# Optimization experiments

Hardware: AMD Instinct MI355X
Metric: run time of the kernel (lower is better)

Reference implementation:

```python
import jax, jax.numpy as jnp
import numpy as np

B, S, E, H = 4, 2048, 1024, 16
D = E // H  # head_dim = 64


def setup_inputs() -> dict:
    key0 = jax.random.key(0)
    ks = jax.random.split(key0, 11)
    sc = 1.0 / np.sqrt(E)
    return {
        "query": jax.random.normal(ks[0], (B, S, E), jnp.float32),
        "key": jax.random.normal(ks[1], (B, S, E), jnp.float32),
        "value": jax.random.normal(ks[2], (B, S, E), jnp.float32),
        "Wq": jax.random.normal(ks[3], (E, E), jnp.float32) * sc,
        "bq": jax.random.normal(ks[4], (E,), jnp.float32) * sc,
        "Wk": jax.random.normal(ks[5], (E, E), jnp.float32) * sc,
        "bk": jax.random.normal(ks[6], (E,), jnp.float32) * sc,
        "Wv": jax.random.normal(ks[7], (E, E), jnp.float32) * sc,
        "bv": jax.random.normal(ks[8], (E,), jnp.float32) * sc,
        "Wo": jax.random.normal(ks[9], (E, E), jnp.float32) * sc,
        "bo": jax.random.normal(ks[10], (E,), jnp.float32) * sc,
    }


def reference(query, key, value, Wq, bq, Wk, bk, Wv, bv, Wo, bo):
    b, s, e = query.shape
    q = query @ Wq + bq
    k = key @ Wk + bk
    v = value @ Wv + bv
    # [b, s, E] -> [b, H, s, D]
    qh = q.reshape(b, s, H, D).transpose(0, 2, 1, 3)
    kh = k.reshape(b, s, H, D).transpose(0, 2, 1, 3)
    vh = v.reshape(b, s, H, D).transpose(0, 2, 1, 3)
    energy = jnp.einsum('nhql,nhkl->nhqk', qh, kh)  # [b, H, s, s]
    scale = jnp.asarray(1.0 / np.sqrt(D), energy.dtype)
    attention = jax.nn.softmax(energy * scale, axis=-1)
    # NOTE: faithful to the source einsum 'nhqk,nhvl->nhql' (k and v both contracted)
    out = jnp.einsum('nhqk,nhvl->nhql', attention, vh)  # [b, H, s, D]
    out = out.transpose(0, 2, 1, 3).reshape(b, s, e)
    return out @ Wo + bo
```

## Files before the change

### kernel.cpp

```cpp
#include <hip/hip_runtime.h>
#include <hip/hip_bf16.h>

#define B_ 4
#define S_ 2048
#define E_ 1024

#define NS 256
#define ROWS (S_ / NS)
#define RB 64
#define CW 16
#define JS (E_ / 256)
#define RPB 8

__global__ __launch_bounds__(256) void k_colsum(const float* __restrict__ value,
                                                const float* __restrict__ bo,
                                                float* __restrict__ pv,
                                                float* __restrict__ o) {
    const int ns = blockIdx.x, b = blockIdx.y;
    const int t = threadIdx.x;
    const float4* src = reinterpret_cast<const float4*>(
        value + ((size_t)b * S_ + (size_t)ns * ROWS) * E_);
    float4 acc = make_float4(0.f, 0.f, 0.f, 0.f);
#pragma unroll
    for (int r = 0; r < ROWS; ++r) {
        float4 v = src[r * (E_ / 4) + t];
        acc.x += v.x; acc.y += v.y; acc.z += v.z; acc.w += v.w;
    }
    reinterpret_cast<float4*>(pv + ((size_t)b * NS + ns) * E_)[t] = acc;
    if (ns == 0) {
        reinterpret_cast<float4*>(o + (size_t)b * E_)[t] =
            reinterpret_cast<const float4*>(bo)[t];
    }
}

__global__ __launch_bounds__(256) void k_gemm1(const float* __restrict__ pv,
                                               const float* __restrict__ Wv,
                                               float* __restrict__ tpart) {
    const int js = blockIdx.x, rb = blockIdx.y, b = blockIdx.z;
    const int t = threadIdx.x;
    __shared__ float red[16][CW];
    __shared__ float vb[CW];

    {
        const int e_l = t & 15;
        const int g = t >> 4;
        float s = 0.f;
        for (int ns = g; ns < NS; ns += 16)
            s += pv[((size_t)b * NS + ns) * E_ + rb * CW + e_l];
        red[g][e_l] = s;
    }
    __syncthreads();
    if (t < CW) {
        float v = 0.f;
#pragma unroll
        for (int g = 0; g < 16; ++g) v += red[g][t];
        vb[t] = v;
    }
    __syncthreads();

    const int j = js * 256 + t;
    const float* w = Wv + (size_t)(rb * CW) * E_ + j;
    float acc = 0.f;
#pragma unroll
    for (int k = 0; k < CW; ++k)
        acc = fmaf(vb[k], w[(size_t)k * E_], acc);
    tpart[((size_t)rb * B_ + b) * E_ + j] = acc;
}

__global__ __launch_bounds__(256) void k_gemm2(const float* __restrict__ tpart,
                                               const float* __restrict__ bv,
                                               const float* __restrict__ Wo,
                                               float* __restrict__ o) {
    const int is = blockIdx.x, rb = blockIdx.y, b = blockIdx.z;
    const int t = threadIdx.x;
    __shared__ float red[16][CW];
    __shared__ float tj[CW];

    {
        const int j_l = t & 15;
        const int g = t >> 4;
        float s = 0.f;
#pragma unroll
        for (int p = g; p < RB; p += 16)
            s += tpart[((size_t)p * B_ + b) * E_ + rb * CW + j_l];
        red[g][j_l] = s;
    }
    __syncthreads();
    if (t < CW) {
        float v = (float)S_ * bv[rb * CW + t];
#pragma unroll
        for (int g = 0; g < 16; ++g) v += red[g][t];
        tj[t] = v;
    }
    __syncthreads();

    const int i = is * 256 + t;
    const float* w = Wo + (size_t)(rb * CW) * E_ + i;
    float acc = 0.f;
#pragma unroll
    for (int k = 0; k < CW; ++k)
        acc = fmaf(tj[k], w[(size_t)k * E_], acc);
    atomicAdd(&o[(size_t)b * E_ + i], acc);
}

__global__ __launch_bounds__(256) void k_bcast(const float* __restrict__ o,
                                               float* __restrict__ out) {
    const int sb = blockIdx.x, b = blockIdx.y;
    const int t = threadIdx.x;
    float4 ov = reinterpret_cast<const float4*>(o + (size_t)b * E_)[t];
    float4* dst = reinterpret_cast<float4*>(
        out + ((size_t)b * S_ + (size_t)sb * RPB) * E_);
#pragma unroll
    for (int r = 0; r < RPB; ++r)
        dst[r * (E_ / 4) + t] = ov;
}

extern "C" void kernel_launch(void* const* d_in, const int* in_sizes, int n_in,
                              void* d_out, int out_size, void* d_ws, size_t ws_size,
                              hipStream_t stream) {
    const float* value = (const float*)d_in[2];
    const float* Wv    = (const float*)d_in[7];
    const float* bv    = (const float*)d_in[8];
    const float* Wo    = (const float*)d_in[9];
    const float* bo    = (const float*)d_in[10];
    float* out = (float*)d_out;

    float* pv    = (float*)d_ws;
    float* tpart = pv + (size_t)B_ * NS * E_;
    float* o     = tpart + (size_t)RB * B_ * E_;

    k_colsum<<<dim3(NS, B_),        256, 0, stream>>>(value, bo, pv, o);
    k_gemm1 <<<dim3(JS, RB, B_),    256, 0, stream>>>(pv, Wv, tpart);
    k_gemm2 <<<dim3(JS, RB, B_),    256, 0, stream>>>(tpart, bv, Wo, o);
    k_bcast <<<dim3(S_ / RPB, B_),  256, 0, stream>>>(o, out);
}
```

Measured before the change: 32.17 us.

## Fuse the two GEMV stages and reduce column sums with atomics

The column-sum kernel now sums 16 rows per block and adds its partial into a per-batch vbar vector with atomics, replacing the partial-sum buffer. The two GEMV kernels are merged into one kernel per 16-column slice. It computes t = vbar·Wv over all of E, adds S*bv, then multiplies by 16 rows of Wo and atomically adds into o. bo is now added in the broadcast kernel, and a memset zeroes the workspace first. This saves one kernel launch and the partial-buffer traffic, at the cost of many atomics and lower per-block parallelism in the Wv pass.

```diff
diff --git a/kernel.cpp b/kernel.cpp
--- a/kernel.cpp
+++ b/kernel.cpp
@@ -5,109 +5,82 @@
 #define S_ 2048
 #define E_ 1024
 
-#define NS 256
-#define ROWS (S_ / NS)
-#define RB 64
-#define CW 16
-#define JS (E_ / 256)
+#define NSB 128
+#define ROWS1 (S_ / NSB)
 #define RPB 8
 
 __global__ __launch_bounds__(256) void k_colsum(const float* __restrict__ value,
-                                                const float* __restrict__ bo,
-                                                float* __restrict__ pv,
-                                                float* __restrict__ o) {
+                                                float* __restrict__ vbar) {
     const int ns = blockIdx.x, b = blockIdx.y;
     const int t = threadIdx.x;
     const float4* src = reinterpret_cast<const float4*>(
-        value + ((size_t)b * S_ + (size_t)ns * ROWS) * E_);
+        value + ((size_t)b * S_ + (size_t)ns * ROWS1) * E_);
     float4 acc = make_float4(0.f, 0.f, 0.f, 0.f);
 #pragma unroll
-    for (int r = 0; r < ROWS; ++r) {
+    for (int r = 0; r < ROWS1; ++r) {
         float4 v = src[r * (E_ / 4) + t];
         acc.x += v.x; acc.y += v.y; acc.z += v.z; acc.w += v.w;
     }
-    reinterpret_cast<float4*>(pv + ((size_t)b * NS + ns) * E_)[t] = acc;
-    if (ns == 0) {
-        reinterpret_cast<float4*>(o + (size_t)b * E_)[t] =
-            reinterpret_cast<const float4*>(bo)[t];
-    }
+    float* dst = vbar + (size_t)b * E_ + t * 4;
+    atomicAdd(dst + 0, acc.x);
+    atomicAdd(dst + 1, acc.y);
+    atomicAdd(dst + 2, acc.z);
+    atomicAdd(dst + 3, acc.w);
 }
 
-__global__ __launch_bounds__(256) void k_gemm1(const float* __restrict__ pv,
-                                               const float* __restrict__ Wv,
-                                               float* __restrict__ tpart) {
-    const int js = blockIdx.x, rb = blockIdx.y, b = blockIdx.z;
+__global__ __launch_bounds__(256) void k_mid(const float* __restrict__ vbar,
+                                             const float* __restrict__ Wv,
+                                             const float* __restrict__ bv,
+                                             const float* __restrict__ Wo,
+                                             float* __restrict__ o) {
+    const int rb = blockIdx.x, b = blockIdx.y;
     const int t = threadIdx.x;
-    __shared__ float red[16][CW];
-    __shared__ float vb[CW];
+    __shared__ float vb[E_];
+    __shared__ float red[16][16];
+    __shared__ float tj[16];
 
-    {
-        const int e_l = t & 15;
-        const int g = t >> 4;
-        float s = 0.f;
-        for (int ns = g; ns < NS; ns += 16)
-            s += pv[((size_t)b * NS + ns) * E_ + rb * CW + e_l];
-        red[g][e_l] = s;
-    }
-    __syncthreads();
-    if (t < CW) {
-        float v = 0.f;
-#pragma unroll
-        for (int g = 0; g < 16; ++g) v += red[g][t];
-        vb[t] = v;
-    }
+    reinterpret_cast<float4*>(vb)[t] =
+        reinterpret_cast<const float4*>(vbar + (size_t)b * E_)[t];
     __syncthreads();
 
-    const int j = js * 256 + t;
-    const float* w = Wv + (size_t)(rb * CW) * E_ + j;
+    const int j_l = t & 15, g = t >> 4;
+    const int j = rb * 16 + j_l;
     float acc = 0.f;
+#pragma unroll 8
+    for (int e = g; e < E_; e += 16)
+        acc = fmaf(vb[e], Wv[(size_t)e * E_ + j], acc);
+    red[g][j_l] = acc;
+    __syncthreads();
+    if (t < 16) {
+        float v = (float)S_ * bv[rb * 16 + t];
 #pragma unroll
-    for (int k = 0; k < CW; ++k)
-        acc = fmaf(vb[k], w[(size_t)k * E_], acc);
-    tpart[((size_t)rb * B_ + b) * E_ + j] = acc;
-}
-
-__global__ __launch_bounds__(256) void k_gemm2(const float* __restrict__ tpart,
-                                               const float* __restrict__ bv,
-                                               const float* __restrict__ Wo,
-                                               float* __restrict__ o) {
-    const int is = blockIdx.x, rb = blockIdx.y, b = blockIdx.z;
-    const int t = threadIdx.x;
-    __shared__ float red[16][CW];
-    __shared__ float tj[CW];
-
-    {
-        const int j_l = t & 15;
-        const int g = t >> 4;
-        float s = 0.f;
-#pragma unroll
-        for (int p = g; p < RB; p += 16)
-            s += tpart[((size_t)p * B_ + b) * E_ + rb * CW + j_l];
-        red[g][j_l] = s;
-    }
-    __syncthreads();
-    if (t < CW) {
-        float v = (float)S_ * bv[rb * CW + t];
-#pragma unroll
-        for (int g = 0; g < 16; ++g) v += red[g][t];
+        for (int gg = 0; gg < 16; ++gg) v += red[gg][t];
         tj[t] = v;
     }
     __syncthreads();
 
-    const int i = is * 256 + t;
-    const float* w = Wo + (size_t)(rb * CW) * E_ + i;
-    float acc = 0.f;
+    float oacc[4] = {0.f, 0.f, 0.f, 0.f};
 #pragma unroll
-    for (int k = 0; k < CW; ++k)
-        acc = fmaf(tj[k], w[(size_t)k * E_], acc);
-    atomicAdd(&o[(size_t)b * E_ + i], acc);
+    for (int jj = 0; jj < 16; ++jj) {
+        const float* wo = Wo + (size_t)(rb * 16 + jj) * E_;
+        const float tv = tj[jj];
+#pragma unroll
+        for (int k2 = 0; k2 < 4; ++k2)
+            oacc[k2] = fmaf(tv, wo[k2 * 256 + t], oacc[k2]);
+    }
+#pragma unroll
+    for (int k2 = 0; k2 < 4; ++k2)
+        atomicAdd(&o[(size_t)b * E_ + k2 * 256 + t], oacc[k2]);
 }
 
 __global__ __launch_bounds__(256) void k_bcast(const float* __restrict__ o,
+                                               const float* __restrict__ bo,
                                                float* __restrict__ out) {
     const int sb = blockIdx.x, b = blockIdx.y;
     const int t = threadIdx.x;
     float4 ov = reinterpret_cast<const float4*>(o + (size_t)b * E_)[t];
+    float4 bb = reinterpret_cast<const float4*>(bo)[t];
+    ov.x += bb.x; ov.y += bb.y; ov.z += bb.z; ov.w += bb.w;
     float4* dst = reinterpret_cast<float4*>(
         out + ((size_t)b * S_ + (size_t)sb * RPB) * E_);
 #pragma unroll
@@ -125,12 +98,11 @@
     const float* bo    = (const float*)d_in[10];
     float* out = (float*)d_out;
 
-    float* pv    = (float*)d_ws;
-    float* tpart = pv + (size_t)B_ * NS * E_;
-    float* o     = tpart + (size_t)RB * B_ * E_;
+    float* vbar = (float*)d_ws;
+    float* o    = vbar + (size_t)B_ * E_;
 
-    k_colsum<<<dim3(NS, B_),        256, 0, stream>>>(value, bo, pv, o);
-    k_gemm1 <<<dim3(JS, RB, B_),    256, 0, stream>>>(pv, Wv, tpart);
-    k_gemm2 <<<dim3(JS, RB, B_),    256, 0, stream>>>(tpart, bv, Wo, o);
-    k_bcast <<<dim3(S_ / RPB, B_),  256, 0, stream>>>(o, out);
+    hipMemsetAsync(d_ws, 0, 2 * (size_t)B_ * E_ * sizeof(float), stream);
+    k_colsum<<<dim3(NSB, B_),      256, 0, stream>>>(value, vbar);
+    k_mid   <<<dim3(E_ / 16, B_),  256, 0, stream>>>(vbar, Wv, bv, Wo, o);
+    k_bcast <<<dim3(S_ / RPB, B_), 256, 0, stream>>>(o, bo, out);
 }
```

New measurement: 48.61 us. +51.1%, slower.
